# Kernel optimization log

Measured on AMD Instinct MI355X. Metric: run time of the kernel, lower is better.

Reference implementation:

```python
import jax, jax.numpy as jnp
import numpy as np

B, T, D, DS, EXP = 1, 2048, 512, 32, 2
EPS = 1e-6


def setup_inputs() -> dict:
    key = jax.random.key(0)
    ks = jax.random.split(key, 16)
    g = lambda k, shape, s: jax.random.normal(k, shape, jnp.float32) * s
    x = jax.random.normal(ks[0], (B, T, D), jnp.float32)
    inv = D ** -0.5
    return {
        "x": x,
        "norm_w": jnp.ones((D,), jnp.float32),
        "W_in": g(ks[1], (D, 2 * D), inv),
        "conv_w": g(ks[2], (D, 1, 4), 0.5),          # depthwise, torch layout (O, I/groups, K)
        "conv_b": g(ks[3], (D,), 0.1),
        "W_dt": g(ks[4], (D, D), 0.01 * inv),
        "b_dt": jnp.full((D,), -8.0, jnp.float32) + g(ks[5], (D,), 0.1),  # Mamba-style small-dt init
        "W_B": g(ks[6], (D, DS), inv),
        "W_C": g(ks[7], (D, DS), inv),
        "W_out": g(ks[8], (D, D), inv),
        "log_A": jnp.log(jnp.linspace(1.0, 16.0, D)).astype(jnp.float32),
        "D_param": jnp.ones((D,), jnp.float32),
        "W_ffn1": g(ks[9], (D, EXP * D), inv),
        "W_ffn2": g(ks[10], (EXP * D, D), (EXP * D) ** -0.5),
        "W_merge": g(ks[11], (2 * D, D), (2 * D) ** -0.5),
    }


def _ssm_scan(xs, dt, Bm, Cm, A):
    # cumsum-based parallel scan, exactly as ParallelSSMScan.forward
    log_a = jnp.clip(dt * A[None, None, :], -20.0, 20.0)      # [B,T,D]
    cum = jnp.cumsum(log_a, axis=1)                            # [B,T,D]
    dtx = dt * xs                                              # [B,T,D]
    inp = dtx[..., None] * Bm[:, :, None, :]                   # [B,T,D,ds]
    scaled = jnp.exp(-cum)[..., None] * inp                    # [B,T,D,ds]
    prefix = jnp.cumsum(scaled, axis=1)                        # [B,T,D,ds]
    h_all = jnp.exp(cum)[..., None] * prefix                   # [B,T,D,ds]
    return jnp.einsum('btds,bts->btd', h_all, Cm)


def _forward(x, norm_w, W_in, conv_w, conv_b, W_dt, b_dt, W_B, W_C, W_out,
             log_A, D_param, W_ffn1, W_ffn2, W_merge):
    r = x
    rms = jnp.sqrt(jnp.mean(x * x, axis=-1, keepdims=True) + EPS)
    xn = x / rms * norm_w
    xz = xn @ W_in
    xs, z = jnp.split(xz, 2, axis=-1)
    # causal depthwise conv (padding=3 then [:T] == left-pad 3, valid)
    xt = jnp.transpose(xs, (0, 2, 1))                          # [B,D,T]
    c = jax.lax.conv_general_dilated(
        xt, conv_w, window_strides=(1,), padding=[(3, 0)],
        feature_group_count=D, dimension_numbers=('NCH', 'OIH', 'NCH'))
    c = c + conv_b[None, :, None]
    xs = jax.nn.silu(jnp.transpose(c, (0, 2, 1)))              # [B,T,D]
    dt = jax.nn.softplus(xs @ W_dt + b_dt)
    Bm = xs @ W_B
    Cm = xs @ W_C
    A = -jnp.exp(log_A)
    y = _ssm_scan(xs, dt, Bm, Cm, A)
    y_ssm = (y + xs * D_param) * jax.nn.silu(z)
    y_ssm = y_ssm @ W_out
    y_ffn = jax.nn.gelu(xn @ W_ffn1, approximate=False) @ W_ffn2
    y = jnp.concatenate([y_ssm, y_ffn], axis=-1) @ W_merge
    # dropout in eval mode -> identity
    return r + y


def reference(x, norm_w, W_in, conv_w, conv_b, W_dt, b_dt, W_B, W_C, W_out,
              log_A, D_param, W_ffn1, W_ffn2, W_merge):
    return _forward(x, norm_w, W_in, conv_w, conv_b, W_dt, b_dt, W_B, W_C,
                    W_out, log_A, D_param, W_ffn1, W_ffn2, W_merge)
```

## Files before the change

kernel.cpp:

```cpp
#include <hip/hip_runtime.h>
#include <math.h>

#define T_LEN 2048
#define D_DIM 512
#define NCHUNK 64
#define CLEN 32

typedef __bf16 bf16x8 __attribute__((ext_vector_type(8)));
typedef float f32x4 __attribute__((ext_vector_type(4)));

__device__ __forceinline__ float silu_f(float x) { return x / (1.f + __expf(-x)); }
__device__ __forceinline__ float softplus_f(float x) {
  return fmaxf(x, 0.f) + log1pf(__expf(-fabsf(x)));
}
__device__ __forceinline__ float gelu_f(float x) {
  return 0.5f * x * (1.f + erff(x * 0.70710678118654752440f));
}
__device__ __forceinline__ unsigned short f2bf(float f) {
  union { float f; unsigned u; } v; v.f = f;
  unsigned r = v.u + 0x7FFF + ((v.u >> 16) & 1);
  return (unsigned short)(r >> 16);
}

__global__ __launch_bounds__(256) void rmsnorm_kernel(
    const float* __restrict__ x, const float* __restrict__ w,
    unsigned short* __restrict__ xn) {
  const int t = blockIdx.x;
  const float2 v = reinterpret_cast<const float2*>(x + (size_t)t * D_DIM)[threadIdx.x];
  float ss = v.x * v.x + v.y * v.y;
#pragma unroll
  for (int m = 1; m < 64; m <<= 1) ss += __shfl_xor(ss, m);
  __shared__ float wsum[4];
  if ((threadIdx.x & 63) == 0) wsum[threadIdx.x >> 6] = ss;
  __syncthreads();
  const float tot = wsum[0] + wsum[1] + wsum[2] + wsum[3];
  const float scale = rsqrtf(tot * (1.f / D_DIM) + 1e-6f);
  const float2 wv = reinterpret_cast<const float2*>(w)[threadIdx.x];
  ushort2 o;
  o.x = f2bf(v.x * scale * wv.x);
  o.y = f2bf(v.y * scale * wv.y);
  reinterpret_cast<ushort2*>(xn + (size_t)t * D_DIM)[threadIdx.x] = o;
}

struct TransJobs {
  const float* src[8];
  unsigned short* dst[8];
  int K[8];
  int N[8];
  int b0[9];
};

__global__ __launch_bounds__(256) void prep_weights_kernel(TransJobs J) {
  __shared__ float tile[32][33];
  const int b = blockIdx.x;
  int ji = 0;
#pragma unroll
  for (int i = 1; i < 8; ++i) ji += (b >= J.b0[i]) ? 1 : 0;
  const float* __restrict__ src = J.src[ji];
  unsigned short* __restrict__ dst = J.dst[ji];
  const int K = J.K[ji], N = J.N[ji];
  const int rel = b - J.b0[ji];
  const int nbx = N >> 5;
  const int bx = rel % nbx, by = rel / nbx;
  const int k0 = by * 32, n0 = bx * 32;
  const int i = threadIdx.x & 31;
  const int r = threadIdx.x >> 5;
#pragma unroll
  for (int p = 0; p < 4; ++p) {
    const int kk = r + p * 8;
    tile[kk][i] = src[(size_t)(k0 + kk) * N + n0 + i];
  }
  __syncthreads();
#pragma unroll
  for (int p = 0; p < 4; ++p) {
    const int nn = r + p * 8;
    dst[(size_t)(n0 + nn) * K + k0 + i] = f2bf(tile[i][nn]);
  }
}

template <int MODE>
__global__ __launch_bounds__(256) void gemm_mfma(
    const unsigned short* __restrict__ Abf, const unsigned short* __restrict__ Btbf,
    void* __restrict__ O1, void* __restrict__ O2, void* __restrict__ O3,
    int M, int N, int K, int ldC,
    const float* __restrict__ bias, const float* __restrict__ resid) {
  __shared__ bf16x8 As[512];
  __shared__ bf16x8 Bs[512];

  const int tid = threadIdx.x;
  const int lane = tid & 63;
  const int w = tid >> 6;
  const int wrow = (w >> 1) * 32;
  const int wcol = (w & 1) * 32;
  const int brow = blockIdx.y * 64;
  const int bcol = blockIdx.x * 64;
  const int K8 = K >> 3;

  const bf16x8* __restrict__ A8 = reinterpret_cast<const bf16x8*>(Abf);
  const bf16x8* __restrict__ B8 = reinterpret_cast<const bf16x8*>(Btbf);

  const int r0s = tid >> 3;
  const int c0s = tid & 7;

  f32x4 acc[2][2];
#pragma unroll
  for (int m = 0; m < 2; ++m)
#pragma unroll
    for (int n = 0; n < 2; ++n) acc[m][n] = {0.f, 0.f, 0.f, 0.f};

  const int nt = K >> 6;
  bf16x8 pa[2], pb[2];
#pragma unroll
  for (int p = 0; p < 2; ++p) {
    const int rr = r0s + p * 32;
    pa[p] = A8[(size_t)(brow + rr) * K8 + c0s];
    pb[p] = B8[(size_t)(bcol + rr) * K8 + c0s];
  }

  for (int t = 0; t < nt; ++t) {
#pragma unroll
    for (int p = 0; p < 2; ++p) {
      const int rr = r0s + p * 32;
      As[rr * 8 + (c0s ^ (rr & 7))] = pa[p];
      Bs[rr * 8 + (c0s ^ (rr & 7))] = pb[p];
    }
    __syncthreads();
    if (t + 1 < nt) {
      const int kb = (t + 1) * 8;
#pragma unroll
      for (int p = 0; p < 2; ++p) {
        const int rr = r0s + p * 32;
        pa[p] = A8[(size_t)(brow + rr) * K8 + kb + c0s];
        pb[p] = B8[(size_t)(bcol + rr) * K8 + kb + c0s];
      }
    }
#pragma unroll
    for (int kk = 0; kk < 2; ++kk) {
      const int slot = kk * 4 + (lane >> 4);
      bf16x8 af[2], bf_[2];
#pragma unroll
      for (int m = 0; m < 2; ++m) {
        const int r = wrow + m * 16 + (lane & 15);
        af[m] = As[r * 8 + (slot ^ (r & 7))];
      }
#pragma unroll
      for (int n = 0; n < 2; ++n) {
        const int r = wcol + n * 16 + (lane & 15);
        bf_[n] = Bs[r * 8 + (slot ^ (r & 7))];
      }
#pragma unroll
      for (int m = 0; m < 2; ++m)
#pragma unroll
        for (int n = 0; n < 2; ++n)
          acc[m][n] = __builtin_amdgcn_mfma_f32_16x16x32_bf16(af[m], bf_[n], acc[m][n], 0, 0, 0);
    }
    __syncthreads();
  }

#pragma unroll
  for (int m = 0; m < 2; ++m) {
#pragma unroll
    for (int n = 0; n < 2; ++n) {
      const int col = bcol + wcol + n * 16 + (lane & 15);
#pragma unroll
      for (int j = 0; j < 4; ++j) {
        const int row = brow + wrow + m * 16 + (lane >> 4) * 4 + j;
        float v = acc[m][n][j];
        if (MODE == 0) {
          if (col < 1024) {
            reinterpret_cast<float*>(O1)[(size_t)row * 1024 + col] = v;
          } else {
            reinterpret_cast<unsigned short*>(O2)[(size_t)row * 1024 + col - 1024] =
                f2bf(gelu_f(v));
          }
        } else if (MODE == 1) {
          if (col < 512) {
            reinterpret_cast<float*>(O1)[(size_t)row * 512 + col] =
                softplus_f(v + bias[col]);
          } else {
            const int s = col - 512;
            float* p = (s < 32) ? reinterpret_cast<float*>(O2)
                                : reinterpret_cast<float*>(O3);
            p[(size_t)row * 32 + (s & 31)] = v;
          }
        } else {
          reinterpret_cast<float*>(O1)[(size_t)row * 512 + col] =
              resid[(size_t)row * 512 + col] + v;
        }
      }
    }
  }
}

__global__ __launch_bounds__(256) void gemm_dual(
    const unsigned short* __restrict__ A0, const unsigned short* __restrict__ B0,
    int K0,
    const unsigned short* __restrict__ A1, const unsigned short* __restrict__ B1,
    int K1, unsigned short* __restrict__ cat) {
  __shared__ bf16x8 As[512];
  __shared__ bf16x8 Bs[512];

  const int z = blockIdx.z;
  const unsigned short* __restrict__ Abf = z ? A1 : A0;
  const unsigned short* __restrict__ Btbf = z ? B1 : B0;
  const int K = z ? K1 : K0;
  unsigned short* __restrict__ outp = cat + (z ? 512 : 0);

  const int tid = threadIdx.x;
  const int lane = tid & 63;
  const int w = tid >> 6;
  const int wrow = (w >> 1) * 32;
  const int wcol = (w & 1) * 32;
  const int brow = blockIdx.y * 64;
  const int bcol = blockIdx.x * 64;
  const int K8 = K >> 3;

  const bf16x8* __restrict__ A8 = reinterpret_cast<const bf16x8*>(Abf);
  const bf16x8* __restrict__ B8 = reinterpret_cast<const bf16x8*>(Btbf);

  const int r0s = tid >> 3;
  const int c0s = tid & 7;

  f32x4 acc[2][2];
#pragma unroll
  for (int m = 0; m < 2; ++m)
#pragma unroll
    for (int n = 0; n < 2; ++n) acc[m][n] = {0.f, 0.f, 0.f, 0.f};

  const int nt = K >> 6;
  bf16x8 pa[2], pb[2];
#pragma unroll
  for (int p = 0; p < 2; ++p) {
    const int rr = r0s + p * 32;
    pa[p] = A8[(size_t)(brow + rr) * K8 + c0s];
    pb[p] = B8[(size_t)(bcol + rr) * K8 + c0s];
  }

  for (int t = 0; t < nt; ++t) {
#pragma unroll
    for (int p = 0; p < 2; ++p) {
      const int rr = r0s + p * 32;
      As[rr * 8 + (c0s ^ (rr & 7))] = pa[p];
      Bs[rr * 8 + (c0s ^ (rr & 7))] = pb[p];
    }
    __syncthreads();
    if (t + 1 < nt) {
      const int kb = (t + 1) * 8;
#pragma unroll
      for (int p = 0; p < 2; ++p) {
        const int rr = r0s + p * 32;
        pa[p] = A8[(size_t)(brow + rr) * K8 + kb + c0s];
        pb[p] = B8[(size_t)(bcol + rr) * K8 + kb + c0s];
      }
    }
#pragma unroll
    for (int kk = 0; kk < 2; ++kk) {
      const int slot = kk * 4 + (lane >> 4);
      bf16x8 af[2], bf_[2];
#pragma unroll
      for (int m = 0; m < 2; ++m) {
        const int r = wrow + m * 16 + (lane & 15);
        af[m] = As[r * 8 + (slot ^ (r & 7))];
      }
#pragma unroll
      for (int n = 0; n < 2; ++n) {
        const int r = wcol + n * 16 + (lane & 15);
        bf_[n] = Bs[r * 8 + (slot ^ (r & 7))];
      }
#pragma unroll
      for (int m = 0; m < 2; ++m)
#pragma unroll
        for (int n = 0; n < 2; ++n)
          acc[m][n] = __builtin_amdgcn_mfma_f32_16x16x32_bf16(af[m], bf_[n], acc[m][n], 0, 0, 0);
    }
    __syncthreads();
  }

#pragma unroll
  for (int m = 0; m < 2; ++m) {
#pragma unroll
    for (int n = 0; n < 2; ++n) {
      const int col = bcol + wcol + n * 16 + (lane & 15);
#pragma unroll
      for (int j = 0; j < 4; ++j) {
        const int row = brow + wrow + m * 16 + (lane >> 4) * 4 + j;
        outp[(size_t)row * 1024 + col] = f2bf(acc[m][n][j]);
      }
    }
  }
}

__global__ __launch_bounds__(256) void conv_silu_kernel(
    const float* __restrict__ xz, const float* __restrict__ cw,
    const float* __restrict__ cb, float* __restrict__ xs,
    unsigned short* __restrict__ xs_bf) {
  const int idx = blockIdx.x * 256 + threadIdx.x;
  const int t = idx >> 9;
  const int d = idx & 511;
  const float4 w = reinterpret_cast<const float4*>(cw)[d];
  float acc = cb[d];
  const float wk[4] = {w.x, w.y, w.z, w.w};
#pragma unroll
  for (int k = 0; k < 4; ++k) {
    const int tt = t - 3 + k;
    if (tt >= 0) acc = fmaf(xz[(size_t)tt * 1024 + d], wk[k], acc);
  }
  const float s = silu_f(acc);
  xs[idx] = s;
  xs_bf[idx] = f2bf(s);
}

__global__ __launch_bounds__(256) void prep_gram_kernel(
    const float* __restrict__ dt, const float* __restrict__ xs,
    const float* __restrict__ Bm, const float* __restrict__ Cm,
    const float* __restrict__ log_A,
    unsigned short* __restrict__ U_T, float* __restrict__ E,
    float* __restrict__ V, float* __restrict__ Pc,
    unsigned short* __restrict__ Gm) {
  __shared__ float4 Bls4[CLEN * 8];
  __shared__ float Bls[32][33], Cls[32][33];

  if (blockIdx.x < 128) {
    const int c = blockIdx.x >> 1;
    const int d = (blockIdx.x & 1) * 256 + threadIdx.x;
    Bls4[threadIdx.x] = reinterpret_cast<const float4*>(Bm + c * CLEN * 32)[threadIdx.x];
    __syncthreads();

    const float A = -__expf(log_A[d]);
    float cum = 0.f;
    float e = 1.f;
    float vacc[32];
#pragma unroll
    for (int s = 0; s < 32; ++s) vacc[s] = 0.f;
    unsigned pk[16];
#pragma unroll
    for (int t = 0; t < CLEN; ++t) {
      const int tg = c * CLEN + t;
      const float dtv = dt[(size_t)tg * D_DIM + d];
      const float xv  = xs[(size_t)tg * D_DIM + d];
      const float la = fminf(fmaxf(dtv * A, -20.f), 20.f);
      cum += la;
      e = __expf(cum);
      E[(size_t)tg * D_DIM + d] = e;
      const float u = __expf(-cum) * dtv * xv;
      const unsigned short ub = f2bf(u);
      if ((t & 1) == 0) pk[t >> 1] = (unsigned)ub;
      else              pk[t >> 1] |= ((unsigned)ub) << 16;
#pragma unroll
      for (int s4 = 0; s4 < 8; ++s4) {
        const float4 b = Bls4[t * 8 + s4];
        vacc[s4 * 4 + 0] = fmaf(u, b.x, vacc[s4 * 4 + 0]);
        vacc[s4 * 4 + 1] = fmaf(u, b.y, vacc[s4 * 4 + 1]);
        vacc[s4 * 4 + 2] = fmaf(u, b.z, vacc[s4 * 4 + 2]);
        vacc[s4 * 4 + 3] = fmaf(u, b.w, vacc[s4 * 4 + 3]);
      }
    }
    {
      uint4* dst = reinterpret_cast<uint4*>(U_T + (size_t)d * T_LEN + c * CLEN);
      dst[0] = make_uint4(pk[0], pk[1], pk[2], pk[3]);
      dst[1] = make_uint4(pk[4], pk[5], pk[6], pk[7]);
      dst[2] = make_uint4(pk[8], pk[9], pk[10], pk[11]);
      dst[3] = make_uint4(pk[12], pk[13], pk[14], pk[15]);
    }
    {
      float4* dst = reinterpret_cast<float4*>(V + ((size_t)c * D_DIM + d) * 32);
#pragma unroll
      for (int s4 = 0; s4 < 8; ++s4)
        dst[s4] = make_float4(vacc[s4 * 4], vacc[s4 * 4 + 1], vacc[s4 * 4 + 2], vacc[s4 * 4 + 3]);
    }
    Pc[c * D_DIM + d] = e;
  } else {
    const int c = blockIdx.x - 128;
    {
      const int t = threadIdx.x >> 3;
      const int s4 = threadIdx.x & 7;
      const float4 b = reinterpret_cast<const float4*>(Bm + (c * CLEN + t) * 32)[s4];
      const float4 cc = reinterpret_cast<const float4*>(Cm + (c * CLEN + t) * 32)[s4];
      Bls[t][s4 * 4 + 0] = b.x;  Bls[t][s4 * 4 + 1] = b.y;
      Bls[t][s4 * 4 + 2] = b.z;  Bls[t][s4 * 4 + 3] = b.w;
      Cls[t][s4 * 4 + 0] = cc.x; Cls[t][s4 * 4 + 1] = cc.y;
      Cls[t][s4 * 4 + 2] = cc.z; Cls[t][s4 * 4 + 3] = cc.w;
    }
    __syncthreads();
    const int t = threadIdx.x >> 3;
    const int tp0 = (threadIdx.x & 7) * 4;
    float g[4];
#pragma unroll
    for (int q = 0; q < 4; ++q) {
      const int tp = tp0 + q;
      float acc = 0.f;
      if (tp <= t) {
#pragma unroll
        for (int s = 0; s < 32; ++s) acc = fmaf(Cls[t][s], Bls[tp][s], acc);
      }
      g[q] = acc;
    }
    ushort4 o;
    o.x = f2bf(g[0]); o.y = f2bf(g[1]); o.z = f2bf(g[2]); o.w = f2bf(g[3]);
    reinterpret_cast<ushort4*>(Gm + c * 1024)[threadIdx.x] = o;
  }
}

__global__ __launch_bounds__(256) void state_scan_kernel(
    const float* __restrict__ V, const float* __restrict__ Pc,
    float* __restrict__ Hin) {
  const int gt = blockIdx.x * 256 + threadIdx.x;
  const int d = gt >> 5;
  float h = 0.f;
  for (int c = 0; c < NCHUNK; ++c) {
    Hin[c * 16384 + gt] = h;
    h = Pc[c * D_DIM + d] * (h + V[c * 16384 + gt]);
  }
}

__global__ __launch_bounds__(256) void ssm_out_kernel(
    const unsigned short* __restrict__ Gm, const unsigned short* __restrict__ U_T,
    const float* __restrict__ Hin, const float* __restrict__ Cm,
    const float* __restrict__ E, const float* __restrict__ xs,
    const float* __restrict__ Dp, const float* __restrict__ xz,
    unsigned short* __restrict__ g) {
  const int c = blockIdx.x;
  const int dt0 = blockIdx.y * 64;
  __shared__ bf16x8 Als[32 * 8];
  __shared__ bf16x8 Bls[64 * 8];
  const int tid = threadIdx.x;

  if (tid < 128) {
    const int t = tid >> 2, q = tid & 3;
    Als[t * 8 + (q ^ (t & 7))] =
        *reinterpret_cast<const bf16x8*>(Gm + c * 1024 + t * 32 + q * 8);
  } else {
    const int i = tid - 128;
    const int t = i >> 2, q = i & 3;
    const float* cp = Cm + (c * CLEN + t) * 32 + q * 8;
    const float4 c0 = *reinterpret_cast<const float4*>(cp);
    const float4 c1 = *reinterpret_cast<const float4*>(cp + 4);
    union { bf16x8 v; unsigned short u[8]; } wv;
    wv.u[0] = f2bf(c0.x); wv.u[1] = f2bf(c0.y); wv.u[2] = f2bf(c0.z); wv.u[3] = f2bf(c0.w);
    wv.u[4] = f2bf(c1.x); wv.u[5] = f2bf(c1.y); wv.u[6] = f2bf(c1.z); wv.u[7] = f2bf(c1.w);
    Als[t * 8 + ((4 + q) ^ (t & 7))] = wv.v;
  }
  {
    const int dd = tid >> 2, q = tid & 3;
    Bls[dd * 8 + (q ^ (dd & 7))] = *reinterpret_cast<const bf16x8*>(
        U_T + (size_t)(dt0 + dd) * T_LEN + c * CLEN + q * 8);
    const float* hp = Hin + ((size_t)c * D_DIM + dt0 + dd) * 32 + q * 8;
    const float4 h0 = *reinterpret_cast<const float4*>(hp);
    const float4 h1 = *reinterpret_cast<const float4*>(hp + 4);
    union { bf16x8 v; unsigned short u[8]; } wv;
    wv.u[0] = f2bf(h0.x); wv.u[1] = f2bf(h0.y); wv.u[2] = f2bf(h0.z); wv.u[3] = f2bf(h0.w);
    wv.u[4] = f2bf(h1.x); wv.u[5] = f2bf(h1.y); wv.u[6] = f2bf(h1.z); wv.u[7] = f2bf(h1.w);
    Bls[dd * 8 + ((4 + q) ^ (dd & 7))] = wv.v;
  }
  __syncthreads();

  const int lane = tid & 63;
  const int w = tid >> 6;
  const int wcol = w * 16;
  f32x4 acc[2];
  acc[0] = {0.f, 0.f, 0.f, 0.f};
  acc[1] = {0.f, 0.f, 0.f, 0.f};
#pragma unroll
  for (int kk = 0; kk < 2; ++kk) {
    const int slot = kk * 4 + (lane >> 4);
    const int rb = wcol + (lane & 15);
    const bf16x8 bfrag = Bls[rb * 8 + (slot ^ (rb & 7))];
#pragma unroll
    for (int m = 0; m < 2; ++m) {
      const int r = m * 16 + (lane & 15);
      const bf16x8 afrag = Als[r * 8 + (slot ^ (r & 7))];
      acc[m] = __builtin_amdgcn_mfma_f32_16x16x32_bf16(afrag, bfrag, acc[m], 0, 0, 0);
    }
  }
  const int dg = dt0 + wcol + (lane & 15);
  const float dpv = Dp[dg];
#pragma unroll
  for (int m = 0; m < 2; ++m) {
#pragma unroll
    for (int j = 0; j < 4; ++j) {
      const int tg = c * CLEN + m * 16 + (lane >> 4) * 4 + j;
      const float y = E[(size_t)tg * D_DIM + dg] * acc[m][j];
      const float xv = xs[(size_t)tg * D_DIM + dg];
      const float zv = xz[(size_t)tg * 1024 + 512 + dg];
      g[(size_t)tg * D_DIM + dg] = f2bf(fmaf(xv, dpv, y) * silu_f(zv));
    }
  }
}

extern "C" void kernel_launch(void* const* d_in, const int* in_sizes, int n_in,
                              void* d_out, int out_size, void* d_ws, size_t ws_size,
                              hipStream_t stream) {
  const float* x      = (const float*)d_in[0];
  const float* norm_w = (const float*)d_in[1];
  const float* W_in   = (const float*)d_in[2];
  const float* conv_w = (const float*)d_in[3];
  const float* conv_b = (const float*)d_in[4];
  const float* W_dt   = (const float*)d_in[5];
  const float* b_dt   = (const float*)d_in[6];
  const float* W_B    = (const float*)d_in[7];
  const float* W_C    = (const float*)d_in[8];
  const float* W_out  = (const float*)d_in[9];
  const float* log_A  = (const float*)d_in[10];
  const float* D_par  = (const float*)d_in[11];
  const float* W_ffn1 = (const float*)d_in[12];
  const float* W_ffn2 = (const float*)d_in[13];
  const float* W_mrg  = (const float*)d_in[14];
  float* out = (float*)d_out;

  const size_t M1 = 1u << 20;
  char* ws = (char*)d_ws;
  size_t off = 0;
  auto alloc_f = [&](size_t n) { float* p = (float*)(ws + off); off += n * 4; return p; };
  auto alloc_h = [&](size_t n) { unsigned short* p = (unsigned short*)(ws + off); off += n * 2; return p; };

  float* xz  = alloc_f(2 * M1);
  float* xs  = alloc_f(M1);
  float* dt  = alloc_f(M1);
  float* E   = alloc_f(M1);
  float* V   = alloc_f(M1);
  float* Hin = alloc_f(M1);
  float* Bm  = alloc_f(1 << 16);
  float* Cm  = alloc_f(1 << 16);
  float* Pc  = alloc_f(NCHUNK * D_DIM);
  unsigned short* U_T    = alloc_h(M1);
  unsigned short* Gm     = alloc_h(NCHUNK * 1024);
  unsigned short* xn_bf  = alloc_h(M1);
  unsigned short* xs_bf  = alloc_h(M1);
  unsigned short* g_bf   = alloc_h(M1);
  unsigned short* h1_bf  = alloc_h(2 * M1);
  unsigned short* cat_bf = alloc_h(2 * M1);
  unsigned short* WinF1T = alloc_h(2048 * 512);
  unsigned short* WdtBCT = alloc_h(576 * 512);
  unsigned short* WoutT  = alloc_h(512 * 512);
  unsigned short* Wf2T   = alloc_h(512 * 1024);
  unsigned short* WmT    = alloc_h(512 * 1024);

  TransJobs J;
  J.src[0] = W_in;   J.dst[0] = WinF1T;              J.K[0] = 512;  J.N[0] = 1024;
  J.src[1] = W_ffn1; J.dst[1] = WinF1T + 1024 * 512; J.K[1] = 512;  J.N[1] = 1024;
  J.src[2] = W_dt;   J.dst[2] = WdtBCT;              J.K[2] = 512;  J.N[2] = 512;
  J.src[3] = W_B;    J.dst[3] = WdtBCT + 512 * 512;  J.K[3] = 512;  J.N[3] = 32;
  J.src[4] = W_C;    J.dst[4] = WdtBCT + 544 * 512;  J.K[4] = 512;  J.N[4] = 32;
  J.src[5] = W_out;  J.dst[5] = WoutT;               J.K[5] = 512;  J.N[5] = 512;
  J.src[6] = W_ffn2; J.dst[6] = Wf2T;                J.K[6] = 1024; J.N[6] = 512;
  J.src[7] = W_mrg;  J.dst[7] = WmT;                 J.K[7] = 1024; J.N[7] = 512;
  int bacc = 0;
  for (int i = 0; i < 8; ++i) {
    J.b0[i] = bacc;
    bacc += (J.N[i] >> 5) * (J.K[i] >> 5);
  }
  J.b0[8] = bacc;
  prep_weights_kernel<<<bacc, 256, 0, stream>>>(J);

  rmsnorm_kernel<<<T_LEN, 256, 0, stream>>>(x, norm_w, xn_bf);
  gemm_mfma<0><<<dim3(32, 32), 256, 0, stream>>>(
      xn_bf, WinF1T, xz, h1_bf, nullptr, 2048, 2048, 512, 0, nullptr, nullptr);
  conv_silu_kernel<<<4096, 256, 0, stream>>>(xz, conv_w, conv_b, xs, xs_bf);
  gemm_mfma<1><<<dim3(9, 32), 256, 0, stream>>>(
      xs_bf, WdtBCT, dt, Bm, Cm, 2048, 576, 512, 0, b_dt, nullptr);
  prep_gram_kernel<<<192, 256, 0, stream>>>(dt, xs, Bm, Cm, log_A, U_T, E, V, Pc, Gm);
  state_scan_kernel<<<64, 256, 0, stream>>>(V, Pc, Hin);
  ssm_out_kernel<<<dim3(NCHUNK, 8), 256, 0, stream>>>(Gm, U_T, Hin, Cm, E, xs, D_par, xz, g_bf);
  gemm_dual<<<dim3(8, 32, 2), 256, 0, stream>>>(
      g_bf, WoutT, 512, h1_bf, Wf2T, 1024, cat_bf);
  gemm_mfma<3><<<dim3(8, 32), 256, 0, stream>>>(
      cat_bf, WmT, out, nullptr, nullptr, 2048, 512, 1024, 0, nullptr, x);
}
```

Before: 90.22 us.

## Fold W_out and W_ffn2 into merge weights and enlarge input GEMM tiles

Precomputes combined weights W_out·W_merge_top and W_ffn2·W_merge_bottom into one 1536-wide matrix. The tail then becomes a single GEMM over the concatenated [g | gelu(h1)] activations, replacing a dual GEMM, an intermediate concat buffer and a separate merge GEMM. The input projection GEMM moves to 128x128 tiles with a 4x4 MFMA accumulator per wave. This saves one launch and activation traffic, but costs a weight-combine kernel each call, a merge GEMM with larger K (1536), and extra bf16 rounding of the combined weights.

```diff
diff --git a/kernel.cpp b/kernel.cpp
--- a/kernel.cpp
+++ b/kernel.cpp
@@ -47,6 +47,7 @@
   unsigned short* dst[8];
   int K[8];
   int N[8];
+  int tr[8];
   int b0[9];
 };
 
@@ -65,58 +66,48 @@
   const int k0 = by * 32, n0 = bx * 32;
   const int i = threadIdx.x & 31;
   const int r = threadIdx.x >> 5;
-#pragma unroll
-  for (int p = 0; p < 4; ++p) {
-    const int kk = r + p * 8;
-    tile[kk][i] = src[(size_t)(k0 + kk) * N + n0 + i];
-  }
-  __syncthreads();
-#pragma unroll
-  for (int p = 0; p < 4; ++p) {
-    const int nn = r + p * 8;
-    dst[(size_t)(n0 + nn) * K + k0 + i] = f2bf(tile[i][nn]);
-  }
-}
-
-template <int MODE>
-__global__ __launch_bounds__(256) void gemm_mfma(
+  if (J.tr[ji]) {
+#pragma unroll
+    for (int p = 0; p < 4; ++p) {
+      const int kk = r + p * 8;
+      tile[kk][i] = src[(size_t)(k0 + kk) * N + n0 + i];
+    }
+    __syncthreads();
+#pragma unroll
+    for (int p = 0; p < 4; ++p) {
+      const int nn = r + p * 8;
+      dst[(size_t)(n0 + nn) * K + k0 + i] = f2bf(tile[i][nn]);
+    }
+  } else {
+#pragma unroll
+    for (int p = 0; p < 4; ++p) {
+      const int kk = r + p * 8;
+      dst[(size_t)(k0 + kk) * N + n0 + i] = f2bf(src[(size_t)(k0 + kk) * N + n0 + i]);
+    }
+  }
+}
+
+__device__ __forceinline__ void gemm64_core(
     const unsigned short* __restrict__ Abf, const unsigned short* __restrict__ Btbf,
-    void* __restrict__ O1, void* __restrict__ O2, void* __restrict__ O3,
-    int M, int N, int K, int ldC,
-    const float* __restrict__ bias, const float* __restrict__ resid) {
-  __shared__ bf16x8 As[512];
-  __shared__ bf16x8 Bs[512];
-
+    int nt, int lda8, int ldb8, int brow, int bcol,
+    bf16x8* __restrict__ As, bf16x8* __restrict__ Bs, f32x4 acc[2][2]) {
   const int tid = threadIdx.x;
   const int lane = tid & 63;
   const int w = tid >> 6;
   const int wrow = (w >> 1) * 32;
   const int wcol = (w & 1) * 32;
-  const int brow = blockIdx.y * 64;
-  const int bcol = blockIdx.x * 64;
-  const int K8 = K >> 3;
-
   const bf16x8* __restrict__ A8 = reinterpret_cast<const bf16x8*>(Abf);
   const bf16x8* __restrict__ B8 = reinterpret_cast<const bf16x8*>(Btbf);
-
   const int r0s = tid >> 3;
   const int c0s = tid & 7;
 
-  f32x4 acc[2][2];
-#pragma unroll
-  for (int m = 0; m < 2; ++m)
-#pragma unroll
-    for (int n = 0; n < 2; ++n) acc[m][n] = {0.f, 0.f, 0.f, 0.f};
-
-  const int nt = K >> 6;
   bf16x8 pa[2], pb[2];
 #pragma unroll
   for (int p = 0; p < 2; ++p) {
     const int rr = r0s + p * 32;
-    pa[p] = A8[(size_t)(brow + rr) * K8 + c0s];
-    pb[p] = B8[(size_t)(bcol + rr) * K8 + c0s];
-  }
-
+    pa[p] = A8[(size_t)(brow + rr) * lda8 + c0s];
+    pb[p] = B8[(size_t)(bcol + rr) * ldb8 + c0s];
+  }
   for (int t = 0; t < nt; ++t) {
 #pragma unroll
     for (int p = 0; p < 2; ++p) {
@@ -130,8 +121,8 @@
 #pragma unroll
       for (int p = 0; p < 2; ++p) {
         const int rr = r0s + p * 32;
-        pa[p] = A8[(size_t)(brow + rr) * K8 + kb + c0s];
-        pb[p] = B8[(size_t)(bcol + rr) * K8 + kb + c0s];
+        pa[p] = A8[(size_t)(brow + rr) * lda8 + kb + c0s];
+        pb[p] = B8[(size_t)(bcol + rr) * ldb8 + kb + c0s];
       }
     }
 #pragma unroll
@@ -156,7 +147,27 @@
     }
     __syncthreads();
   }
-
+}
+
+__global__ __launch_bounds__(256) void gemm64_dtbc(
+    const unsigned short* __restrict__ Abf, const unsigned short* __restrict__ Btbf,
+    float* __restrict__ dt, float* __restrict__ Bm, float* __restrict__ Cm,
+    const float* __restrict__ bias) {
+  __shared__ bf16x8 As[512];
+  __shared__ bf16x8 Bs[512];
+  f32x4 acc[2][2];
+#pragma unroll
+  for (int m = 0; m < 2; ++m)
+#pragma unroll
+    for (int n = 0; n < 2; ++n) acc[m][n] = {0.f, 0.f, 0.f, 0.f};
+  const int brow = blockIdx.y * 64;
+  const int bcol = blockIdx.x * 64;
+  gemm64_core(Abf, Btbf, 8, 64, 64, brow, bcol, As, Bs, acc);
+
+  const int lane = threadIdx.x & 63;
+  const int w = threadIdx.x >> 6;
+  const int wrow = (w >> 1) * 32;
+  const int wcol = (w & 1) * 32;
 #pragma unroll
   for (int m = 0; m < 2; ++m) {
 #pragma unroll
@@ -165,126 +176,174 @@
 #pragma unroll
       for (int j = 0; j < 4; ++j) {
         const int row = brow + wrow + m * 16 + (lane >> 4) * 4 + j;
-        float v = acc[m][n][j];
-        if (MODE == 0) {
-          if (col < 1024) {
-            reinterpret_cast<float*>(O1)[(size_t)row * 1024 + col] = v;
-          } else {
-            reinterpret_cast<unsigned short*>(O2)[(size_t)row * 1024 + col - 1024] =
-                f2bf(gelu_f(v));
-          }
-        } else if (MODE == 1) {
-          if (col < 512) {
-            reinterpret_cast<float*>(O1)[(size_t)row * 512 + col] =
-                softplus_f(v + bias[col]);
-          } else {
-            const int s = col - 512;
-            float* p = (s < 32) ? reinterpret_cast<float*>(O2)
-                                : reinterpret_cast<float*>(O3);
-            p[(size_t)row * 32 + (s & 31)] = v;
-          }
+        const float v = acc[m][n][j];
+        if (col < 512) {
+          dt[(size_t)row * 512 + col] = softplus_f(v + bias[col]);
         } else {
-          reinterpret_cast<float*>(O1)[(size_t)row * 512 + col] =
-              resid[(size_t)row * 512 + col] + v;
+          const int s = col - 512;
+          float* p = (s < 32) ? Bm : Cm;
+          p[(size_t)row * 32 + (s & 31)] = v;
         }
       }
     }
   }
 }
 
-__global__ __launch_bounds__(256) void gemm_dual(
-    const unsigned short* __restrict__ A0, const unsigned short* __restrict__ B0,
-    int K0,
-    const unsigned short* __restrict__ A1, const unsigned short* __restrict__ B1,
-    int K1, unsigned short* __restrict__ cat) {
+__global__ __launch_bounds__(256) void combine_kernel(
+    const unsigned short* __restrict__ WmT, const unsigned short* __restrict__ WoutBF,
+    const unsigned short* __restrict__ Wf2BF, unsigned short* __restrict__ WcombT) {
+  const int z = blockIdx.z;
+  if (z == 0 && blockIdx.x >= 8) return;
   __shared__ bf16x8 As[512];
   __shared__ bf16x8 Bs[512];
-
-  const int z = blockIdx.z;
-  const unsigned short* __restrict__ Abf = z ? A1 : A0;
-  const unsigned short* __restrict__ Btbf = z ? B1 : B0;
-  const int K = z ? K1 : K0;
-  unsigned short* __restrict__ outp = cat + (z ? 512 : 0);
-
+  const unsigned short* A = z ? (WmT + 512) : WmT;
+  const unsigned short* Bt = z ? Wf2BF : WoutBF;
+  const int coff = z ? 512 : 0;
+  f32x4 acc[2][2];
+#pragma unroll
+  for (int m = 0; m < 2; ++m)
+#pragma unroll
+    for (int n = 0; n < 2; ++n) acc[m][n] = {0.f, 0.f, 0.f, 0.f};
+  const int brow = blockIdx.y * 64;
+  const int bcol = blockIdx.x * 64;
+  gemm64_core(A, Bt, 8, 128, 64, brow, bcol, As, Bs, acc);
+
+  const int lane = threadIdx.x & 63;
+  const int w = threadIdx.x >> 6;
+  const int wrow = (w >> 1) * 32;
+  const int wcol = (w & 1) * 32;
+#pragma unroll
+  for (int m = 0; m < 2; ++m) {
+#pragma unroll
+    for (int n = 0; n < 2; ++n) {
+      const int col = bcol + wcol + n * 16 + (lane & 15);
+#pragma unroll
+      for (int j = 0; j < 4; ++j) {
+        const int row = brow + wrow + m * 16 + (lane >> 4) * 4 + j;
+        WcombT[(size_t)row * 1536 + coff + col] = f2bf(acc[m][n][j]);
+      }
+    }
+  }
+}
+
+__global__ __launch_bounds__(256) void gemm64_merge(
+    const unsigned short* __restrict__ Abf, const unsigned short* __restrict__ Btbf,
+    float* __restrict__ out, const float* __restrict__ resid) {
+  __shared__ bf16x8 As[512];
+  __shared__ bf16x8 Bs[512];
+  f32x4 acc[2][2];
+#pragma unroll
+  for (int m = 0; m < 2; ++m)
+#pragma unroll
+    for (int n = 0; n < 2; ++n) acc[m][n] = {0.f, 0.f, 0.f, 0.f};
+  const int brow = blockIdx.y * 64;
+  const int bcol = blockIdx.x * 64;
+  gemm64_core(Abf, Btbf, 24, 192, 192, brow, bcol, As, Bs, acc);
+
+  const int lane = threadIdx.x & 63;
+  const int w = threadIdx.x >> 6;
+  const int wrow = (w >> 1) * 32;
+  const int wcol = (w & 1) * 32;
+#pragma unroll
+  for (int m = 0; m < 2; ++m) {
+#pragma unroll
+    for (int n = 0; n < 2; ++n) {
+      const int col = bcol + wcol + n * 16 + (lane & 15);
+#pragma unroll
+      for (int j = 0; j < 4; ++j) {
+        const int row = brow + wrow + m * 16 + (lane >> 4) * 4 + j;
+        out[(size_t)row * 512 + col] = resid[(size_t)row * 512 + col] + acc[m][n][j];
+      }
+    }
+  }
+}
+
+__global__ __launch_bounds__(256) void gemm128_in(
+    const unsigned short* __restrict__ Abf, const unsigned short* __restrict__ Btbf,
+    float* __restrict__ xz, unsigned short* __restrict__ comb) {
+  __shared__ bf16x8 As[1024];
+  __shared__ bf16x8 Bs[1024];
   const int tid = threadIdx.x;
   const int lane = tid & 63;
   const int w = tid >> 6;
-  const int wrow = (w >> 1) * 32;
-  const int wcol = (w & 1) * 32;
-  const int brow = blockIdx.y * 64;
-  const int bcol = blockIdx.x * 64;
-  const int K8 = K >> 3;
+  const int wrow = (w >> 1) * 64;
+  const int wcol = (w & 1) * 64;
+  const int brow = blockIdx.y * 128;
+  const int bcol = blockIdx.x * 128;
+  const int K8 = 64;
 
   const bf16x8* __restrict__ A8 = reinterpret_cast<const bf16x8*>(Abf);
   const bf16x8* __restrict__ B8 = reinterpret_cast<const bf16x8*>(Btbf);
 
-  const int r0s = tid >> 3;
-  const int c0s = tid & 7;
-
-  f32x4 acc[2][2];
-#pragma unroll
-  for (int m = 0; m < 2; ++m)
-#pragma unroll
-    for (int n = 0; n < 2; ++n) acc[m][n] = {0.f, 0.f, 0.f, 0.f};
-
-  const int nt = K >> 6;
-  bf16x8 pa[2], pb[2];
-#pragma unroll
-  for (int p = 0; p < 2; ++p) {
-    const int rr = r0s + p * 32;
-    pa[p] = A8[(size_t)(brow + rr) * K8 + c0s];
-    pb[p] = B8[(size_t)(bcol + rr) * K8 + c0s];
-  }
-
-  for (int t = 0; t < nt; ++t) {
-#pragma unroll
-    for (int p = 0; p < 2; ++p) {
-      const int rr = r0s + p * 32;
-      As[rr * 8 + (c0s ^ (rr & 7))] = pa[p];
-      Bs[rr * 8 + (c0s ^ (rr & 7))] = pb[p];
+  f32x4 acc[4][4];
+#pragma unroll
+  for (int m = 0; m < 4; ++m)
+#pragma unroll
+    for (int n = 0; n < 4; ++n) acc[m][n] = {0.f, 0.f, 0.f, 0.f};
+
+  const int slot = tid & 7;
+  bf16x8 pa[4], pb[4];
+#pragma unroll
+  for (int p = 0; p < 4; ++p) {
+    const int row = p * 32 + (tid >> 3);
+    pa[p] = A8[(size_t)(brow + row) * K8 + slot];
+    pb[p] = B8[(size_t)(bcol + row) * K8 + slot];
+  }
+
+  for (int t = 0; t < 8; ++t) {
+#pragma unroll
+    for (int p = 0; p < 4; ++p) {
+      const int row = p * 32 + (tid >> 3);
+      As[row * 8 + (slot ^ (row & 7))] = pa[p];
+      Bs[row * 8 + (slot ^ (row & 7))] = pb[p];
     }
     __syncthreads();
-    if (t + 1 < nt) {
+    if (t + 1 < 8) {
       const int kb = (t + 1) * 8;
 #pragma unroll
-      for (int p = 0; p < 2; ++p) {
-        const int rr = r0s + p * 32;
-        pa[p] = A8[(size_t)(brow + rr) * K8 + kb + c0s];
-        pb[p] = B8[(size_t)(bcol + rr) * K8 + kb + c0s];
+      for (int p = 0; p < 4; ++p) {
+        const int row = p * 32 + (tid >> 3);
+        pa[p] = A8[(size_t)(brow + row) * K8 + kb + slot];
+        pb[p] = B8[(size_t)(bcol + row) * K8 + kb + slot];
       }
     }
 #pragma unroll
     for (int kk = 0; kk < 2; ++kk) {
-      const int slot = kk * 4 + (lane >> 4);
-      bf16x8 af[2], bf_[2];
-#pragma unroll
-      for (int m = 0; m < 2; ++m) {
+      const int q = kk * 4 + (lane >> 4);
+      bf16x8 af[4], bf_[4];
+#pragma unroll
+      for (int m = 0; m < 4; ++m) {
         const int r = wrow + m * 16 + (lane & 15);
-        af[m] = As[r * 8 + (slot ^ (r & 7))];
-      }
-#pragma unroll
-      for (int n = 0; n < 2; ++n) {
+        af[m] = As[r * 8 + (q ^ (r & 7))];
+      }
+#pragma unroll
+      for (int n = 0; n < 4; ++n) {
         const int r = wcol + n * 16 + (lane & 15);
-        bf_[n] = Bs[r * 8 + (slot ^ (r & 7))];
-      }
-#pragma unroll
-      for (int m = 0; m < 2; ++m)
-#pragma unroll
-        for (int n = 0; n < 2; ++n)
+        bf_[n] = Bs[r * 8 + (q ^ (r & 7))];
+      }
+#pragma unroll
+      for (int m = 0; m < 4; ++m)
+#pragma unroll
+        for (int n = 0; n < 4; ++n)
           acc[m][n] = __builtin_amdgcn_mfma_f32_16x16x32_bf16(af[m], bf_[n], acc[m][n], 0, 0, 0);
     }
     __syncthreads();
   }
 
 #pragma unroll
-  for (int m = 0; m < 2; ++m) {
-#pragma unroll
-    for (int n = 0; n < 2; ++n) {
+  for (int m = 0; m < 4; ++m) {
+#pragma unroll
+    for (int n = 0; n < 4; ++n) {
       const int col = bcol + wcol + n * 16 + (lane & 15);
 #pragma unroll
       for (int j = 0; j < 4; ++j) {
         const int row = brow + wrow + m * 16 + (lane >> 4) * 4 + j;
-        outp[(size_t)row * 1024 + col] = f2bf(acc[m][n][j]);
+        const float v = acc[m][n][j];
+        if (col < 1024) {
+          xz[(size_t)row * 1024 + col] = v;
+        } else {
+          comb[(size_t)row * 1536 + 512 + (col - 1024)] = f2bf(gelu_f(v));
+        }
       }
     }
   }
@@ -418,7 +477,7 @@
     const float* __restrict__ Hin, const float* __restrict__ Cm,
     const float* __restrict__ E, const float* __restrict__ xs,
     const float* __restrict__ Dp, const float* __restrict__ xz,
-    unsigned short* __restrict__ g) {
+    unsigned short* __restrict__ comb) {
   const int c = blockIdx.x;
   const int dt0 = blockIdx.y * 64;
   __shared__ bf16x8 Als[32 * 8];
@@ -482,7 +541,7 @@
       const float y = E[(size_t)tg * D_DIM + dg] * acc[m][j];
       const float xv = xs[(size_t)tg * D_DIM + dg];
       const float zv = xz[(size_t)tg * 1024 + 512 + dg];
-      g[(size_t)tg * D_DIM + dg] = f2bf(fmaf(xv, dpv, y) * silu_f(zv));
+      comb[(size_t)tg * 1536 + dg] = f2bf(fmaf(xv, dpv, y) * silu_f(zv));
     }
   }
 }
@@ -526,24 +585,23 @@
   unsigned short* Gm     = alloc_h(NCHUNK * 1024);
   unsigned short* xn_bf  = alloc_h(M1);
   unsigned short* xs_bf  = alloc_h(M1);
-  unsigned short* g_bf   = alloc_h(M1);
-  unsigned short* h1_bf  = alloc_h(2 * M1);
-  unsigned short* cat_bf = alloc_h(2 * M1);
+  unsigned short* comb   = alloc_h(2048 * 1536);
   unsigned short* WinF1T = alloc_h(2048 * 512);
   unsigned short* WdtBCT = alloc_h(576 * 512);
-  unsigned short* WoutT  = alloc_h(512 * 512);
-  unsigned short* Wf2T   = alloc_h(512 * 1024);
   unsigned short* WmT    = alloc_h(512 * 1024);
+  unsigned short* WoutBF = alloc_h(512 * 512);
+  unsigned short* Wf2BF  = alloc_h(1024 * 512);
+  unsigned short* WcombT = alloc_h(512 * 1536);
 
   TransJobs J;
-  J.src[0] = W_in;   J.dst[0] = WinF1T;              J.K[0] = 512;  J.N[0] = 1024;
-  J.src[1] = W_ffn1; J.dst[1] = WinF1T + 1024 * 512; J.K[1] = 512;  J.N[1] = 1024;
-  J.src[2] = W_dt;   J.dst[2] = WdtBCT;              J.K[2] = 512;  J.N[2] = 512;
-  J.src[3] = W_B;    J.dst[3] = WdtBCT + 512 * 512;  J.K[3] = 512;  J.N[3] = 32;
-  J.src[4] = W_C;    J.dst[4] = WdtBCT + 544 * 512;  J.K[4] = 512;  J.N[4] = 32;
-  J.src[5] = W_out;  J.dst[5] = WoutT;               J.K[5] = 512;  J.N[5] = 512;
-  J.src[6] = W_ffn2; J.dst[6] = Wf2T;                J.K[6] = 1024; J.N[6] = 512;
-  J.src[7] = W_mrg;  J.dst[7] = WmT;                 J.K[7] = 1024; J.N[7] = 512;
+  J.src[0] = W_in;   J.dst[0] = WinF1T;              J.K[0] = 512;  J.N[0] = 1024; J.tr[0] = 1;
+  J.src[1] = W_ffn1; J.dst[1] = WinF1T + 1024 * 512; J.K[1] = 512;  J.N[1] = 1024; J.tr[1] = 1;
+  J.src[2] = W_dt;   J.dst[2] = WdtBCT;              J.K[2] = 512;  J.N[2] = 512;  J.tr[2] = 1;
+  J.src[3] = W_B;    J.dst[3] = WdtBCT + 512 * 512;  J.K[3] = 512;  J.N[3] = 32;   J.tr[3] = 1;
+  J.src[4] = W_C;    J.dst[4] = WdtBCT + 544 * 512;  J.K[4] = 512;  J.N[4] = 32;   J.tr[4] = 1;
+  J.src[5] = W_mrg;  J.dst[5] = WmT;                 J.K[5] = 1024; J.N[5] = 512;  J.tr[5] = 1;
+  J.src[6] = W_out;  J.dst[6] = WoutBF;              J.K[6] = 512;  J.N[6] = 512;  J.tr[6] = 0;
+  J.src[7] = W_ffn2; J.dst[7] = Wf2BF;               J.K[7] = 1024; J.N[7] = 512;  J.tr[7] = 0;
   int bacc = 0;
   for (int i = 0; i < 8; ++i) {
     J.b0[i] = bacc;
@@ -552,17 +610,14 @@
   J.b0[8] = bacc;
   prep_weights_kernel<<<bacc, 256, 0, stream>>>(J);
 
+  combine_kernel<<<dim3(16, 8, 2), 256, 0, stream>>>(WmT, WoutBF, Wf2BF, WcombT);
+
   rmsnorm_kernel<<<T_LEN, 256, 0, stream>>>(x, norm_w, xn_bf);
-  gemm_mfma<0><<<dim3(32, 32), 256, 0, stream>>>(
-      xn_bf, WinF1T, xz, h1_bf, nullptr, 2048, 2048, 512, 0, nullptr, nullptr);
+  gemm128_in<<<dim3(16, 16), 256, 0, stream>>>(xn_bf, WinF1T, xz, comb);
   conv_silu_kernel<<<4096, 256, 0, stream>>>(xz, conv_w, conv_b, xs, xs_bf);
-  gemm_mfma<1><<<dim3(9, 32), 256, 0, stream>>>(
-      xs_bf, WdtBCT, dt, Bm, Cm, 2048, 576, 512, 0, b_dt, nullptr);
+  gemm64_dtbc<<<dim3(9, 32), 256, 0, stream>>>(xs_bf, WdtBCT, dt, Bm, Cm, b_dt);
   prep_gram_kernel<<<192, 256, 0, stream>>>(dt, xs, Bm, Cm, log_A, U_T, E, V, Pc, Gm);
   state_scan_kernel<<<64, 256, 0, stream>>>(V, Pc, Hin);
-  ssm_out_kernel<<<dim3(NCHUNK, 8), 256, 0, stream>>>(Gm, U_T, Hin, Cm, E, xs, D_par, xz, g_bf);
-  gemm_dual<<<dim3(8, 32, 2), 256, 0, stream>>>(
-      g_bf, WoutT, 512, h1_bf, Wf2T, 1024, cat_bf);
-  gemm_mfma<3><<<dim3(8, 32), 256, 0, stream>>>(
-      cat_bf, WmT, out, nullptr, nullptr, 2048, 512, 1024, 0, nullptr, x);
-}
+  ssm_out_kernel<<<dim3(NCHUNK, 8), 256, 0, stream>>>(Gm, U_T, Hin, Cm, E, xs, D_par, xz, comb);
+  gemm64_merge<<<dim3(8, 32), 256, 0, stream>>>(comb, WcombT, out, x);
+}
```

Result: slower. 135.9 us (+50.6%).
